# Optimization experiments

Measured on AMD Instinct MI355X. Metric: run time of the kernel, lower is better.

The kernel has to match this reference:

```python
import jax, jax.numpy as jnp
import numpy as np

B, T, C = 1, 3072, 1024
H, KVH, HD = 16, 4, 64
HI, DI = 16, 32
LOCAL = 128
TOP_K = max(int(T * 0.5), LOCAL)  # 1536
EPS = 1.1920929e-07  # torch fp32 finfo eps used by F.rms_norm
NEG = -1.0e9
POS = 1.0e9


def _rope(x, cos, sin):
    d = x.shape[-1] // 2
    x1, x2 = x[..., :d], x[..., d:]
    return jnp.concatenate([x1 * cos + x2 * sin, -x1 * sin + x2 * cos], axis=-1)


def _rms(x):
    return x * jax.lax.rsqrt(jnp.mean(x * x, axis=-1, keepdims=True) + EPS)


def setup_inputs() -> dict:
    key = jax.random.key(0)
    ks = jax.random.split(key, 10)
    s = 0.02
    return {
        "x": jax.random.normal(ks[0], (B, T, C), jnp.float32),
        "cos": jax.random.uniform(ks[1], (1, T, 1, HD // 2), jnp.float32),
        "sin": jax.random.uniform(ks[2], (1, T, 1, HD // 2), jnp.float32),
        "Wq": jax.random.normal(ks[3], (C, H * HD), jnp.float32) * s,
        "Wk": jax.random.normal(ks[4], (C, KVH * HD), jnp.float32) * s,
        "Wv": jax.random.normal(ks[5], (C, KVH * HD), jnp.float32) * s,
        "Wo": jax.random.normal(ks[6], (C, C), jnp.float32) * s,
        "Wiq": jax.random.normal(ks[7], (C, HI * DI), jnp.float32) * s,
        "Wik": jax.random.normal(ks[8], (C, DI), jnp.float32) * s,
        "Wiw": jax.random.normal(ks[9], (C, HI), jnp.float32) * s,
    }


def reference(x, cos, sin, Wq, Wk, Wv, Wo, Wiq, Wik, Wiw):
    # projections
    q = (x @ Wq).reshape(B, T, H, HD)
    k = (x @ Wk).reshape(B, T, KVH, HD)
    v = (x @ Wv).reshape(B, T, KVH, HD)
    q, k = _rope(q, cos, sin), _rope(k, cos, sin)
    q, k = _rms(q), _rms(k)

    # lightning indexer: I(t,s) = sum_h w(t,h) * relu(q_I(t,h).k_I(s))
    iq = (x @ Wiq).reshape(B, T, HI, DI)
    ik = x @ Wik  # (B,T,DI)
    iw = x @ Wiw  # (B,T,HI)
    sc = jax.nn.relu(jnp.einsum('bqhd,bkd->bqhk', iq, ik))
    imp = jnp.einsum('bqh,bqhk->bqk', iw, sc)  # (B,T,T)

    pos = jnp.arange(T)
    causal = (pos[None, :] > pos[:, None])  # True where key s > query t
    dist = pos[None, :] - pos[:, None]
    in_local = (dist >= 0) & (dist < LOCAL)
    imp = jnp.where(causal[None], NEG, imp)
    imp = jnp.where(in_local[None], POS, imp)

    # hard top-k mask
    _, top_idx = jax.lax.top_k(imp, TOP_K)  # (B,T,K)
    bi = jnp.arange(B)[:, None, None]
    ti = jnp.arange(T)[None, :, None]
    hard = jnp.zeros((B, T, T), x.dtype).at[bi, ti, top_idx].set(1.0)
    causal_f = causal.astype(x.dtype)[None]
    hard = hard * (1.0 - causal_f)
    di = jnp.arange(T)
    hard = hard.at[:, di, di].set(1.0)

    # straight-through sigmoid gate
    soft = jax.nn.sigmoid(imp * 0.1) * (1.0 - causal_f)
    soft = soft.at[:, di, di].set(1.0)
    gate = soft + jax.lax.stop_gradient(hard - soft)
    attn_bias = jnp.log(jnp.clip(gate, 1e-6))[:, None]  # (B,1,T,T)

    # GQA attention with additive bias
    rep = H // KVH
    qs = q.transpose(0, 2, 1, 3)                        # (B,H,T,HD)
    ks_ = jnp.repeat(k.transpose(0, 2, 1, 3), rep, axis=1)
    vs = jnp.repeat(v.transpose(0, 2, 1, 3), rep, axis=1)
    scale = 1.0 / np.sqrt(HD)
    logits = jnp.einsum('bhqd,bhkd->bhqk', qs, ks_) * scale + attn_bias
    att = jax.nn.softmax(logits, axis=-1)
    y = jnp.einsum('bhqk,bhkd->bhqd', att, vs)
    y = y.transpose(0, 2, 1, 3).reshape(B, T, C)
    return y @ Wo
```

## Files before the change

### kernel.cpp

```cpp
#include <hip/hip_runtime.h>
#include <hip/hip_bf16.h>
#include <math.h>

#define T_SEQ   3072
#define C_DIM   1024
#define NH      16
#define NKV     4
#define HD      64
#define HI      16
#define DI      32
#define LOCAL_W 128
#define TOPK    1536
#define SELQ0   (TOPK - LOCAL_W + 1)
#define RMS_EPS 1.1920929e-07f
#define LOGEPS  -13.815510558f
#define SCALE   0.125f
#define MASKW   (T_SEQ / 32)
#define QKVI_N  2176
#define IQ_OFF  1536
#define IK_OFF  2048
#define IW_OFF  2080

typedef __bf16 bf16_t;
typedef __bf16 bf16x8 __attribute__((ext_vector_type(8)));
typedef float  f32x4  __attribute__((ext_vector_type(4)));

__global__ __launch_bounds__(256) void transp_conv(const float* __restrict__ W,
                                                   bf16_t* __restrict__ Wt, int N) {
    __shared__ float t[64][65];
    int n0 = blockIdx.x * 64, k0 = blockIdx.y * 64;
#pragma unroll
    for (int it = 0; it < 16; ++it) {
        int flat = it * 256 + threadIdx.x;
        int i = flat >> 6, j = flat & 63;
        t[i][j] = W[(size_t)(k0 + i) * N + n0 + j];
    }
    __syncthreads();
#pragma unroll
    for (int it = 0; it < 16; ++it) {
        int flat = it * 256 + threadIdx.x;
        int n = flat >> 6, kk = flat & 63;
        Wt[(size_t)(n0 + n) * 1024 + k0 + kk] = (bf16_t)t[kk][n];
    }
}

__global__ __launch_bounds__(256) void transp_conv_g(const float* __restrict__ W,
                                                     bf16_t* __restrict__ Wt, int N) {
    __shared__ float t[64][65];
    int k0 = blockIdx.y * 64;
#pragma unroll
    for (int it = 0; it < 16; ++it) {
        int flat = it * 256 + threadIdx.x;
        int i = flat >> 6, j = flat & 63;
        t[i][j] = (j < N) ? W[(size_t)(k0 + i) * N + j] : 0.f;
    }
    __syncthreads();
#pragma unroll
    for (int it = 0; it < 16; ++it) {
        int flat = it * 256 + threadIdx.x;
        int n = flat >> 6, kk = flat & 63;
        if (n < N) Wt[(size_t)n * 1024 + k0 + kk] = (bf16_t)t[kk][n];
    }
}

__global__ __launch_bounds__(256) void transp_v(const float* __restrict__ qkvi,
                                                bf16_t* __restrict__ Vtg) {
    __shared__ float t[64][65];
    int t0 = blockIdx.x * 64, kvh = blockIdx.y;
#pragma unroll
    for (int it = 0; it < 16; ++it) {
        int flat = it * 256 + threadIdx.x;
        int i = flat >> 6, j = flat & 63;
        t[i][j] = qkvi[(size_t)(t0 + i) * QKVI_N + 1280 + kvh * HD + j];
    }
    __syncthreads();
#pragma unroll
    for (int it = 0; it < 16; ++it) {
        int flat = it * 256 + threadIdx.x;
        int dd = flat >> 6, tt = flat & 63;
        Vtg[(size_t)(kvh * HD + dd) * T_SEQ + t0 + tt] = (bf16_t)t[tt][dd];
    }
}

template<bool A_F32>
__global__ __launch_bounds__(256) void gemm_mfma_t(const void* __restrict__ Ap,
                                                   const bf16_t* __restrict__ Bt,
                                                   float* __restrict__ C, int N) {
    __shared__ __align__(16) bf16_t As[128 * 64];
    __shared__ __align__(16) bf16_t Bs[128 * 64];
    const int tid = threadIdx.x;
    const int m0 = blockIdx.y * 128, n0 = blockIdx.x * 128;
    const int wid = tid >> 6, lane = tid & 63;
    const int wr = wid >> 1, wc = wid & 1;
    const int fr = lane & 15, fq = lane >> 4;

    f32x4 acc[4][4];
#pragma unroll
    for (int i = 0; i < 4; ++i)
#pragma unroll
        for (int j = 0; j < 4; ++j) acc[i][j] = (f32x4){0.f, 0.f, 0.f, 0.f};

    for (int k0 = 0; k0 < 1024; k0 += 64) {
        __syncthreads();
#pragma unroll
        for (int s = tid; s < 1024; s += 256) {
            int row = s >> 3, slot = s & 7;
            int sw = slot ^ (row & 7);
            bf16x8 av;
            if constexpr (A_F32) {
                const float* A = (const float*)Ap;
                const float* src = &A[(size_t)(m0 + row) * 1024 + k0 + slot * 8];
                float4 a = *reinterpret_cast<const float4*>(src);
                float4 b = *reinterpret_cast<const float4*>(src + 4);
                av[0] = (bf16_t)a.x; av[1] = (bf16_t)a.y; av[2] = (bf16_t)a.z; av[3] = (bf16_t)a.w;
                av[4] = (bf16_t)b.x; av[5] = (bf16_t)b.y; av[6] = (bf16_t)b.z; av[7] = (bf16_t)b.w;
            } else {
                const bf16_t* A = (const bf16_t*)Ap;
                av = *reinterpret_cast<const bf16x8*>(&A[(size_t)(m0 + row) * 1024 + k0 + slot * 8]);
            }
            *reinterpret_cast<bf16x8*>(&As[row * 64 + sw * 8]) = av;
            bf16x8 bv = *reinterpret_cast<const bf16x8*>(&Bt[(size_t)(n0 + row) * 1024 + k0 + slot * 8]);
            *reinterpret_cast<bf16x8*>(&Bs[row * 64 + sw * 8]) = bv;
        }
        __syncthreads();
#pragma unroll
        for (int kk = 0; kk < 2; ++kk) {
            bf16x8 af[4], bfr[4];
#pragma unroll
            for (int i = 0; i < 4; ++i) {
                int arow = wr * 64 + i * 16 + fr;
                int aslot = (kk * 4 + fq) ^ (arow & 7);
                af[i] = *reinterpret_cast<const bf16x8*>(&As[arow * 64 + aslot * 8]);
                int brow = wc * 64 + i * 16 + fr;
                int bslot = (kk * 4 + fq) ^ (brow & 7);
                bfr[i] = *reinterpret_cast<const bf16x8*>(&Bs[brow * 64 + bslot * 8]);
            }
#pragma unroll
            for (int i = 0; i < 4; ++i)
#pragma unroll
                for (int j = 0; j < 4; ++j)
                    acc[i][j] = __builtin_amdgcn_mfma_f32_16x16x32_bf16(af[i], bfr[j], acc[i][j], 0, 0, 0);
        }
    }
#pragma unroll
    for (int i = 0; i < 4; ++i)
#pragma unroll
        for (int j = 0; j < 4; ++j)
#pragma unroll
            for (int r = 0; r < 4; ++r) {
                int row = m0 + wr * 64 + i * 16 + fq * 4 + r;
                int col = n0 + wc * 64 + j * 16 + fr;
                C[(size_t)row * N + col] = acc[i][j][r];
            }
}

__global__ __launch_bounds__(256) void rope_rms(float* __restrict__ data,
                                                const float* __restrict__ cosb,
                                                const float* __restrict__ sinb,
                                                int nheads, int rowstride, int coloff) {
    int idx = blockIdx.x * blockDim.x + threadIdx.x;
    if (idx >= T_SEQ * nheads) return;
    int t = idx / nheads, hh = idx % nheads;
    float* p = data + (size_t)t * rowstride + coloff + hh * HD;
    float o[HD];
    float ss = 0.f;
#pragma unroll
    for (int d = 0; d < 32; ++d) {
        float x1 = p[d], x2 = p[d + 32];
        float c = cosb[t * 32 + d], s = sinb[t * 32 + d];
        float a = x1 * c + x2 * s;
        float b = x2 * c - x1 * s;
        o[d] = a; o[d + 32] = b;
        ss += a * a + b * b;
    }
    float r = 1.0f / sqrtf(ss * (1.0f / HD) + RMS_EPS);
#pragma unroll
    for (int d = 0; d < HD; ++d) p[d] = o[d] * r;
}

__global__ __launch_bounds__(256) void imp_select(const float* __restrict__ qkvi,
                                                  unsigned* __restrict__ selmask) {
    const int q = SELQ0 + blockIdx.x;
    const int tid = threadIdx.x;
    const int wid = tid >> 6, lane = tid & 63;
    const int fr = lane & 15, fq = lane >> 4;

    __shared__ unsigned keys[T_SEQ];
    __shared__ unsigned hist[256];
    __shared__ int sufx[257];
    __shared__ unsigned gtw[MASKW], eqw[MASKW];
    __shared__ int s_digit, s_need;

    const float* iqp = &qkvi[(size_t)q * QKVI_N + IQ_OFF + fr * DI + fq * 8];
    float4 qa = *reinterpret_cast<const float4*>(iqp);
    float4 qb = *reinterpret_cast<const float4*>(iqp + 4);
    bf16x8 bq;
    bq[0] = (bf16_t)qa.x; bq[1] = (bf16_t)qa.y; bq[2] = (bf16_t)qa.z; bq[3] = (bf16_t)qa.w;
    bq[4] = (bf16_t)qb.x; bq[5] = (bf16_t)qb.y; bq[6] = (bf16_t)qb.z; bq[7] = (bf16_t)qb.w;
    const float wh = qkvi[(size_t)q * QKVI_N + IW_OFF + fr];

    for (int k0 = 0; k0 < q; k0 += 64) {
        int krow = k0 + wid * 16 + fr;
        const float* ikp = &qkvi[(size_t)krow * QKVI_N + IK_OFF + fq * 8];
        float4 a = *reinterpret_cast<const float4*>(ikp);
        float4 b = *reinterpret_cast<const float4*>(ikp + 4);
        bf16x8 ak;
        ak[0] = (bf16_t)a.x; ak[1] = (bf16_t)a.y; ak[2] = (bf16_t)a.z; ak[3] = (bf16_t)a.w;
        ak[4] = (bf16_t)b.x; ak[5] = (bf16_t)b.y; ak[6] = (bf16_t)b.z; ak[7] = (bf16_t)b.w;
        f32x4 c = (f32x4){0.f, 0.f, 0.f, 0.f};
        c = __builtin_amdgcn_mfma_f32_16x16x32_bf16(ak, bq, c, 0, 0, 0);
        float p0 = wh * fmaxf(c[0], 0.f);
        float p1 = wh * fmaxf(c[1], 0.f);
        float p2 = wh * fmaxf(c[2], 0.f);
        float p3 = wh * fmaxf(c[3], 0.f);
#pragma unroll
        for (int m = 1; m < 16; m <<= 1) {
            p0 += __shfl_xor(p0, m);
            p1 += __shfl_xor(p1, m);
            p2 += __shfl_xor(p2, m);
            p3 += __shfl_xor(p3, m);
        }
        if (fr == 0) {
            int kb = k0 + wid * 16 + fq * 4;
            float pv[4] = {p0, p1, p2, p3};
#pragma unroll
            for (int r = 0; r < 4; ++r) {
                int k = kb + r;
                if (k < q) {
                    unsigned u = __float_as_uint(pv[r]);
                    keys[k] = (u & 0x80000000u) ? ~u : (u | 0x80000000u);
                }
            }
        }
    }
    __syncthreads();

    const int F = min(LOCAL_W, T_SEQ - q);
    int need = TOPK - F;
    unsigned pref = 0;
    for (int b = 3; b >= 0; --b) {
        hist[tid] = 0;
        __syncthreads();
        unsigned above = (b == 3) ? 0u : (~0u << ((b + 1) * 8));
        for (int k = tid; k < q; k += 256) {
            unsigned key = keys[k];
            if ((key & above) == (pref & above))
                atomicAdd(&hist[(key >> (b * 8)) & 255u], 1u);
        }
        __syncthreads();
        sufx[tid] = (int)hist[tid];
        if (tid == 0) sufx[256] = 0;
        __syncthreads();
        for (int s = 1; s < 256; s <<= 1) {
            int v = sufx[tid] + ((tid + s < 256) ? sufx[tid + s] : 0);
            __syncthreads();
            sufx[tid] = v;
            __syncthreads();
        }
        int nxt = sufx[tid + 1];
        if (sufx[tid] >= need && nxt < need) { s_digit = tid; s_need = need - nxt; }
        __syncthreads();
        pref |= ((unsigned)s_digit) << (b * 8);
        need = s_need;
        __syncthreads();
    }
    const unsigned V = pref;
    const int slots = need;

    for (int w = tid; w < MASKW; w += 256) {
        unsigned g = 0, e = 0;
        int kbase = w * 32;
#pragma unroll 4
        for (int bit = 0; bit < 32; ++bit) {
            int k = kbase + bit;
            if (k < q) {
                unsigned key = keys[k];
                if (key > V) g |= (1u << bit);
                else if (key == V) e |= (1u << bit);
            }
        }
        gtw[w] = g; eqw[w] = e;
    }
    __syncthreads();
    if (tid == 0) {
        int rem = slots;
        for (int w = 0; w < MASKW && rem > 0; ++w) {
            unsigned e = eqw[w];
            if (!e) continue;
            int pc = __popc(e);
            if (pc <= rem) { gtw[w] |= e; rem -= pc; }
            else {
                unsigned sel = 0;
                for (int i = 0; i < rem; ++i) { unsigned lb = e & (~e + 1u); sel |= lb; e ^= lb; }
                gtw[w] |= sel; rem = 0;
            }
        }
    }
    __syncthreads();
    for (int w = tid; w < MASKW; w += 256) selmask[(size_t)q * MASKW + w] = gtw[w];
}

__global__ __launch_bounds__(256) void attn_mfma(const float* __restrict__ qkvi,
                                                 const bf16_t* __restrict__ Vtg,
                                                 const unsigned* __restrict__ selmask,
                                                 float* __restrict__ yb) {
    const int q0 = blockIdx.x * 64;
    const int h = blockIdx.y;
    const int kvh = h >> 2;
    const int tid = threadIdx.x;
    const int wid = tid >> 6, lane = tid & 63;
    const int fr = lane & 15, fq = lane >> 4;

    __shared__ __align__(16) bf16_t Qs[64 * 64];
    __shared__ __align__(16) bf16_t Ks[64 * 64];
    __shared__ __align__(16) bf16_t Vts[64 * 64];
    __shared__ __align__(16) float Sb[64][68];
    __shared__ float mrow[64], lrow[64], arow[64];

#pragma unroll
    for (int it = 0; it < 2; ++it) {
        int s = it * 256 + tid;
        int row = s >> 3, slot = s & 7;
        const float* src = &qkvi[(size_t)(q0 + row) * QKVI_N + h * HD + slot * 8];
        float4 a = *reinterpret_cast<const float4*>(src);
        float4 b = *reinterpret_cast<const float4*>(src + 4);
        bf16x8 v;
        v[0] = (bf16_t)(a.x * SCALE); v[1] = (bf16_t)(a.y * SCALE);
        v[2] = (bf16_t)(a.z * SCALE); v[3] = (bf16_t)(a.w * SCALE);
        v[4] = (bf16_t)(b.x * SCALE); v[5] = (bf16_t)(b.y * SCALE);
        v[6] = (bf16_t)(b.z * SCALE); v[7] = (bf16_t)(b.w * SCALE);
        *reinterpret_cast<bf16x8*>(&Qs[row * 64 + (slot ^ (row & 7)) * 8]) = v;
    }
    if (tid < 64) { mrow[tid] = -1e30f; lrow[tid] = 0.f; }

    f32x4 oc[4];
#pragma unroll
    for (int j = 0; j < 4; ++j) oc[j] = (f32x4){0.f, 0.f, 0.f, 0.f};
    __syncthreads();

    for (int k0 = 0; k0 < T_SEQ; k0 += 64) {
#pragma unroll
        for (int it = 0; it < 2; ++it) {
            int s = it * 256 + tid;
            int row = s >> 3, slot = s & 7;
            const float* src = &qkvi[(size_t)(k0 + row) * QKVI_N + 1024 + kvh * HD + slot * 8];
            float4 a = *reinterpret_cast<const float4*>(src);
            float4 b = *reinterpret_cast<const float4*>(src + 4);
            bf16x8 v;
            v[0] = (bf16_t)a.x; v[1] = (bf16_t)a.y; v[2] = (bf16_t)a.z; v[3] = (bf16_t)a.w;
            v[4] = (bf16_t)b.x; v[5] = (bf16_t)b.y; v[6] = (bf16_t)b.z; v[7] = (bf16_t)b.w;
            *reinterpret_cast<bf16x8*>(&Ks[row * 64 + (slot ^ (row & 7)) * 8]) = v;
            *reinterpret_cast<bf16x8*>(&Vts[row * 64 + (slot ^ (row & 7)) * 8]) =
                *reinterpret_cast<const bf16x8*>(&Vtg[(size_t)(kvh * HD + row) * T_SEQ + k0 + slot * 8]);
        }
        __syncthreads();

        f32x4 sacc[4];
#pragma unroll
        for (int j = 0; j < 4; ++j) sacc[j] = (f32x4){0.f, 0.f, 0.f, 0.f};
#pragma unroll
        for (int kc = 0; kc < 2; ++kc) {
            int arow_ = wid * 16 + fr;
            bf16x8 aq = *reinterpret_cast<const bf16x8*>(&Qs[arow_ * 64 + (((kc * 4 + fq) ^ (arow_ & 7))) * 8]);
#pragma unroll
            for (int jb = 0; jb < 4; ++jb) {
                int brow = jb * 16 + fr;
                bf16x8 bk = *reinterpret_cast<const bf16x8*>(&Ks[brow * 64 + (((kc * 4 + fq) ^ (brow & 7))) * 8]);
                sacc[jb] = __builtin_amdgcn_mfma_f32_16x16x32_bf16(aq, bk, sacc[jb], 0, 0, 0);
            }
        }
#pragma unroll
        for (int jb = 0; jb < 4; ++jb)
#pragma unroll
            for (int r = 0; r < 4; ++r) {
                int qq = q0 + wid * 16 + fq * 4 + r;
                int kk = k0 + jb * 16 + fr;
                float bias;
                if (kk == qq) bias = 0.f;
                else if (kk > qq) bias = LOGEPS;
                else if (qq < SELQ0) bias = 0.f;
                else bias = ((selmask[(size_t)qq * MASKW + (kk >> 5)] >> (kk & 31)) & 1u) ? 0.f : LOGEPS;
                Sb[wid * 16 + fq * 4 + r][jb * 16 + fr] = sacc[jb][r] + bias;
            }
        __syncthreads();

        {
            int r = tid >> 2, ln = tid & 3;
            float mx = -1e30f;
#pragma unroll
            for (int c = 0; c < 16; ++c) mx = fmaxf(mx, Sb[r][ln * 16 + c]);
            mx = fmaxf(mx, __shfl_xor(mx, 1, 64));
            mx = fmaxf(mx, __shfl_xor(mx, 2, 64));
            float mnew = fmaxf(mrow[r], mx);
            float ssum = 0.f;
#pragma unroll
            for (int c = 0; c < 16; ++c) {
                float p = __expf(Sb[r][ln * 16 + c] - mnew);
                Sb[r][ln * 16 + c] = p;
                ssum += p;
            }
            ssum += __shfl_xor(ssum, 1, 64);
            ssum += __shfl_xor(ssum, 2, 64);
            if (ln == 0) {
                float a = __expf(mrow[r] - mnew);
                lrow[r] = lrow[r] * a + ssum;
                mrow[r] = mnew;
                arow[r] = a;
            }
        }
        __syncthreads();

#pragma unroll
        for (int r = 0; r < 4; ++r) {
            float a = arow[wid * 16 + fq * 4 + r];
#pragma unroll
            for (int jb = 0; jb < 4; ++jb) oc[jb][r] *= a;
        }
#pragma unroll
        for (int kc = 0; kc < 2; ++kc) {
            const float* ps = &Sb[wid * 16 + fr][kc * 32 + fq * 8];
            float4 p0 = *reinterpret_cast<const float4*>(ps);
            float4 p1 = *reinterpret_cast<const float4*>(ps + 4);
            bf16x8 ap;
            ap[0] = (bf16_t)p0.x; ap[1] = (bf16_t)p0.y; ap[2] = (bf16_t)p0.z; ap[3] = (bf16_t)p0.w;
            ap[4] = (bf16_t)p1.x; ap[5] = (bf16_t)p1.y; ap[6] = (bf16_t)p1.z; ap[7] = (bf16_t)p1.w;
#pragma unroll
            for (int jb = 0; jb < 4; ++jb) {
                int brow = jb * 16 + fr;
                bf16x8 bv = *reinterpret_cast<const bf16x8*>(&Vts[brow * 64 + (((kc * 4 + fq) ^ (brow & 7))) * 8]);
                oc[jb] = __builtin_amdgcn_mfma_f32_16x16x32_bf16(ap, bv, oc[jb], 0, 0, 0);
            }
        }
        __syncthreads();
    }

#pragma unroll
    for (int r = 0; r < 4; ++r) {
        int rowl = wid * 16 + fq * 4 + r;
        float inv = 1.0f / lrow[rowl];
#pragma unroll
        for (int jb = 0; jb < 4; ++jb)
            yb[(size_t)(q0 + rowl) * C_DIM + h * HD + jb * 16 + fr] = oc[jb][r] * inv;
    }
}

extern "C" void kernel_launch(void* const* d_in, const int* in_sizes, int n_in,
                              void* d_out, int out_size, void* d_ws, size_t ws_size,
                              hipStream_t stream) {
    const float* x    = (const float*)d_in[0];
    const float* cosb = (const float*)d_in[1];
    const float* sinb = (const float*)d_in[2];
    const float* Wq   = (const float*)d_in[3];
    const float* Wk   = (const float*)d_in[4];
    const float* Wv   = (const float*)d_in[5];
    const float* Wo   = (const float*)d_in[6];
    const float* Wiq  = (const float*)d_in[7];
    const float* Wik  = (const float*)d_in[8];
    const float* Wiw  = (const float*)d_in[9];
    float* out = (float*)d_out;

    char* cur = (char*)d_ws;
    auto carve = [&](size_t bytes) { char* p = cur; cur += (bytes + 255) & ~(size_t)255; return p; };
    float*    qkvi  = (float*)   carve((size_t)T_SEQ * QKVI_N * 4);
    float*    yb    = (float*)   carve((size_t)T_SEQ * C_DIM * 4);
    unsigned* selm  = (unsigned*)carve((size_t)T_SEQ * MASKW * 4);
    bf16_t*   Wtp   = (bf16_t*)  carve((size_t)QKVI_N * C_DIM * 2);
    bf16_t*   Wot   = (bf16_t*)  carve((size_t)C_DIM * C_DIM * 2);
    bf16_t*   Vtg   = (bf16_t*)  carve((size_t)NKV * HD * T_SEQ * 2);
    if ((size_t)(cur - (char*)d_ws) > ws_size) return;

    dim3 blk(256);

    transp_conv<<<dim3(16, 16), blk, 0, stream>>>(Wq,  Wtp + (size_t)0    * 1024, 1024);
    transp_conv<<<dim3(4, 16),  blk, 0, stream>>>(Wk,  Wtp + (size_t)1024 * 1024, 256);
    transp_conv<<<dim3(4, 16),  blk, 0, stream>>>(Wv,  Wtp + (size_t)1280 * 1024, 256);
    transp_conv<<<dim3(8, 16),  blk, 0, stream>>>(Wiq, Wtp + (size_t)IQ_OFF * 1024, 512);
    transp_conv_g<<<dim3(1, 16), blk, 0, stream>>>(Wik, Wtp + (size_t)IK_OFF * 1024, DI);
    transp_conv_g<<<dim3(1, 16), blk, 0, stream>>>(Wiw, Wtp + (size_t)IW_OFF * 1024, HI);
    transp_conv<<<dim3(16, 16), blk, 0, stream>>>(Wo,  Wot, 1024);

    gemm_mfma_t<true><<<dim3(QKVI_N / 128, T_SEQ / 128), blk, 0, stream>>>(x, Wtp, qkvi, QKVI_N);

    rope_rms<<<(T_SEQ * NH + 255) / 256, blk, 0, stream>>>(qkvi, cosb, sinb, NH, QKVI_N, 0);
    rope_rms<<<(T_SEQ * NKV + 255) / 256, blk, 0, stream>>>(qkvi, cosb, sinb, NKV, QKVI_N, 1024);
    transp_v<<<dim3(T_SEQ / 64, NKV), blk, 0, stream>>>(qkvi, Vtg);

    imp_select<<<T_SEQ - SELQ0, blk, 0, stream>>>(qkvi, selm);

    attn_mfma<<<dim3(T_SEQ / 64, NH), blk, 0, stream>>>(qkvi, Vtg, selm, yb);

    gemm_mfma_t<true><<<dim3(C_DIM / 128, T_SEQ / 128), blk, 0, stream>>>(yb, Wot, out, C_DIM);
}
```

Baseline: 517.0 us.

## Precompute bf16 K and full causal bitmask; stage mask words in LDS

K is converted to bf16 once in a packing kernel instead of being reloaded as fp32 and converted in every attention block. A new kernel writes causal/local bitmask rows for early queries, and imp_select sets the diagonal bit, so attention reads one precomputed mask per tile into LDS rather than branching per element with global loads. Softmax row processing uses float4 LDS accesses. This adds an extra kernel launch and workspace for the bf16 K copy and mask rows.

```diff
diff --git a/kernel.cpp b/kernel.cpp
--- a/kernel.cpp
+++ b/kernel.cpp
@@ -63,10 +63,23 @@
     }
 }
 
-__global__ __launch_bounds__(256) void transp_v(const float* __restrict__ qkvi,
-                                                bf16_t* __restrict__ Vtg) {
+__global__ __launch_bounds__(256) void pack_kv(const float* __restrict__ qkvi,
+                                               bf16_t* __restrict__ Kb,
+                                               bf16_t* __restrict__ Vtg) {
     __shared__ float t[64][65];
     int t0 = blockIdx.x * 64, kvh = blockIdx.y;
+#pragma unroll
+    for (int it = 0; it < 2; ++it) {
+        int s = it * 256 + threadIdx.x;
+        int row = s >> 3, slot = s & 7;
+        const float* src = &qkvi[(size_t)(t0 + row) * QKVI_N + 1024 + kvh * HD + slot * 8];
+        float4 a = *reinterpret_cast<const float4*>(src);
+        float4 b = *reinterpret_cast<const float4*>(src + 4);
+        bf16x8 v;
+        v[0] = (bf16_t)a.x; v[1] = (bf16_t)a.y; v[2] = (bf16_t)a.z; v[3] = (bf16_t)a.w;
+        v[4] = (bf16_t)b.x; v[5] = (bf16_t)b.y; v[6] = (bf16_t)b.z; v[7] = (bf16_t)b.w;
+        *reinterpret_cast<bf16x8*>(&Kb[(size_t)(t0 + row) * (NKV * HD) + kvh * HD + slot * 8]) = v;
+    }
 #pragma unroll
     for (int it = 0; it < 16; ++it) {
         int flat = it * 256 + threadIdx.x;
@@ -80,6 +93,18 @@
         int dd = flat >> 6, tt = flat & 63;
         Vtg[(size_t)(kvh * HD + dd) * T_SEQ + t0 + tt] = (bf16_t)t[tt][dd];
     }
+}
+
+__global__ __launch_bounds__(256) void causal_mask(unsigned* __restrict__ selm) {
+    int idx = blockIdx.x * 256 + threadIdx.x;
+    if (idx >= SELQ0 * MASKW) return;
+    int row = idx / MASKW, w = idx % MASKW;
+    int wq = row >> 5, b = row & 31;
+    unsigned v;
+    if (w < wq) v = ~0u;
+    else if (w == wq) v = (b == 31) ? ~0u : ((1u << (b + 1)) - 1u);
+    else v = 0u;
+    selm[(size_t)row * MASKW + w] = v;
 }
 
 template<bool A_F32>
@@ -297,10 +322,15 @@
         }
     }
     __syncthreads();
-    for (int w = tid; w < MASKW; w += 256) selmask[(size_t)q * MASKW + w] = gtw[w];
+    for (int w = tid; w < MASKW; w += 256) {
+        unsigned g = gtw[w];
+        if (w == (q >> 5)) g |= (1u << (q & 31));
+        selmask[(size_t)q * MASKW + w] = g;
+    }
 }
 
 __global__ __launch_bounds__(256) void attn_mfma(const float* __restrict__ qkvi,
+                                                 const bf16_t* __restrict__ Kb,
                                                  const bf16_t* __restrict__ Vtg,
                                                  const unsigned* __restrict__ selmask,
                                                  float* __restrict__ yb) {
@@ -315,6 +345,7 @@
     __shared__ __align__(16) bf16_t Ks[64 * 64];
     __shared__ __align__(16) bf16_t Vts[64 * 64];
     __shared__ __align__(16) float Sb[64][68];
+    __shared__ unsigned mlds[64][2];
     __shared__ float mrow[64], lrow[64], arow[64];
 
 #pragma unroll
@@ -343,15 +374,14 @@
         for (int it = 0; it < 2; ++it) {
             int s = it * 256 + tid;
             int row = s >> 3, slot = s & 7;
-            const float* src = &qkvi[(size_t)(k0 + row) * QKVI_N + 1024 + kvh * HD + slot * 8];
-            float4 a = *reinterpret_cast<const float4*>(src);
-            float4 b = *reinterpret_cast<const float4*>(src + 4);
-            bf16x8 v;
-            v[0] = (bf16_t)a.x; v[1] = (bf16_t)a.y; v[2] = (bf16_t)a.z; v[3] = (bf16_t)a.w;
-            v[4] = (bf16_t)b.x; v[5] = (bf16_t)b.y; v[6] = (bf16_t)b.z; v[7] = (bf16_t)b.w;
-            *reinterpret_cast<bf16x8*>(&Ks[row * 64 + (slot ^ (row & 7)) * 8]) = v;
+            *reinterpret_cast<bf16x8*>(&Ks[row * 64 + (slot ^ (row & 7)) * 8]) =
+                *reinterpret_cast<const bf16x8*>(&Kb[(size_t)(k0 + row) * (NKV * HD) + kvh * HD + slot * 8]);
             *reinterpret_cast<bf16x8*>(&Vts[row * 64 + (slot ^ (row & 7)) * 8]) =
                 *reinterpret_cast<const bf16x8*>(&Vtg[(size_t)(kvh * HD + row) * T_SEQ + k0 + slot * 8]);
+        }
+        if (tid < 128) {
+            int row = tid >> 1, w = tid & 1;
+            mlds[row][w] = selmask[(size_t)(q0 + row) * MASKW + (k0 >> 5) + w];
         }
         __syncthreads();
 
@@ -373,32 +403,34 @@
         for (int jb = 0; jb < 4; ++jb)
 #pragma unroll
             for (int r = 0; r < 4; ++r) {
-                int qq = q0 + wid * 16 + fq * 4 + r;
-                int kk = k0 + jb * 16 + fr;
-                float bias;
-                if (kk == qq) bias = 0.f;
-                else if (kk > qq) bias = LOGEPS;
-                else if (qq < SELQ0) bias = 0.f;
-                else bias = ((selmask[(size_t)qq * MASKW + (kk >> 5)] >> (kk & 31)) & 1u) ? 0.f : LOGEPS;
+                unsigned mw = mlds[wid * 16 + fq * 4 + r][jb >> 1];
+                float bias = ((mw >> ((jb & 1) * 16 + fr)) & 1u) ? 0.f : LOGEPS;
                 Sb[wid * 16 + fq * 4 + r][jb * 16 + fr] = sacc[jb][r] + bias;
             }
         __syncthreads();
 
         {
             int r = tid >> 2, ln = tid & 3;
-            float mx = -1e30f;
-#pragma unroll
-            for (int c = 0; c < 16; ++c) mx = fmaxf(mx, Sb[r][ln * 16 + c]);
+            float4* sp = reinterpret_cast<float4*>(&Sb[r][ln * 16]);
+            float4 v0 = sp[0], v1 = sp[1], v2 = sp[2], v3 = sp[3];
+            float mx = fmaxf(fmaxf(fmaxf(v0.x, v0.y), fmaxf(v0.z, v0.w)),
+                             fmaxf(fmaxf(v1.x, v1.y), fmaxf(v1.z, v1.w)));
+            mx = fmaxf(mx, fmaxf(fmaxf(fmaxf(v2.x, v2.y), fmaxf(v2.z, v2.w)),
+                                 fmaxf(fmaxf(v3.x, v3.y), fmaxf(v3.z, v3.w))));
             mx = fmaxf(mx, __shfl_xor(mx, 1, 64));
             mx = fmaxf(mx, __shfl_xor(mx, 2, 64));
             float mnew = fmaxf(mrow[r], mx);
-            float ssum = 0.f;
-#pragma unroll
-            for (int c = 0; c < 16; ++c) {
-                float p = __expf(Sb[r][ln * 16 + c] - mnew);
-                Sb[r][ln * 16 + c] = p;
-                ssum += p;
-            }
+            v0.x = __expf(v0.x - mnew); v0.y = __expf(v0.y - mnew);
+            v0.z = __expf(v0.z - mnew); v0.w = __expf(v0.w - mnew);
+            v1.x = __expf(v1.x - mnew); v1.y = __expf(v1.y - mnew);
+            v1.z = __expf(v1.z - mnew); v1.w = __expf(v1.w - mnew);
+            v2.x = __expf(v2.x - mnew); v2.y = __expf(v2.y - mnew);
+            v2.z = __expf(v2.z - mnew); v2.w = __expf(v2.w - mnew);
+            v3.x = __expf(v3.x - mnew); v3.y = __expf(v3.y - mnew);
+            v3.z = __expf(v3.z - mnew); v3.w = __expf(v3.w - mnew);
+            float ssum = (v0.x + v0.y + v0.z + v0.w) + (v1.x + v1.y + v1.z + v1.w)
+                       + (v2.x + v2.y + v2.z + v2.w) + (v3.x + v3.y + v3.z + v3.w);
+            sp[0] = v0; sp[1] = v1; sp[2] = v2; sp[3] = v3;
             ssum += __shfl_xor(ssum, 1, 64);
             ssum += __shfl_xor(ssum, 2, 64);
             if (ln == 0) {
@@ -467,6 +499,7 @@
     bf16_t*   Wtp   = (bf16_t*)  carve((size_t)QKVI_N * C_DIM * 2);
     bf16_t*   Wot   = (bf16_t*)  carve((size_t)C_DIM * C_DIM * 2);
     bf16_t*   Vtg   = (bf16_t*)  carve((size_t)NKV * HD * T_SEQ * 2);
+    bf16_t*   Kb16  = (bf16_t*)  carve((size_t)T_SEQ * NKV * HD * 2);
     if ((size_t)(cur - (char*)d_ws) > ws_size) return;
 
     dim3 blk(256);
@@ -480,14 +513,15 @@
     transp_conv<<<dim3(16, 16), blk, 0, stream>>>(Wo,  Wot, 1024);
 
     gemm_mfma_t<true><<<dim3(QKVI_N / 128, T_SEQ / 128), blk, 0, stream>>>(x, Wtp, qkvi, QKVI_N);
+    causal_mask<<<(SELQ0 * MASKW + 255) / 256, blk, 0, stream>>>(selm);
 
     rope_rms<<<(T_SEQ * NH + 255) / 256, blk, 0, stream>>>(qkvi, cosb, sinb, NH, QKVI_N, 0);
     rope_rms<<<(T_SEQ * NKV + 255) / 256, blk, 0, stream>>>(qkvi, cosb, sinb, NKV, QKVI_N, 1024);
-    transp_v<<<dim3(T_SEQ / 64, NKV), blk, 0, stream>>>(qkvi, Vtg);
+    pack_kv<<<dim3(T_SEQ / 64, NKV), blk, 0, stream>>>(qkvi, Kb16, Vtg);
 
     imp_select<<<T_SEQ - SELQ0, blk, 0, stream>>>(qkvi, selm);
 
-    attn_mfma<<<dim3(T_SEQ / 64, NH), blk, 0, stream>>>(qkvi, Vtg, selm, yb);
+    attn_mfma<<<dim3(T_SEQ / 64, NH), blk, 0, stream>>>(qkvi, Kb16, Vtg, selm, yb);
 
     gemm_mfma_t<true><<<dim3(C_DIM / 128, T_SEQ / 128), blk, 0, stream>>>(yb, Wot, out, C_DIM);
 }
```

New measurement: 429.7 us. -16.9%, faster.
